# Kernel tuning notes

Hardware: AMD Instinct MI355X
Metric: run time of the kernel (lower is better)

Reference implementation:

```python
import jax, jax.numpy as jnp
import numpy as np
import math

B, S, D, H = 4, 2048, 512, 8
DK = D // H


def setup_inputs() -> dict:
    key = jax.random.key(0)
    ks = jax.random.split(key, 12)
    def lin(k, scale):
        return jax.random.normal(k, (D, D), dtype=jnp.float32) * scale
    s = 1.0 / math.sqrt(D)
    return {
        "q": jax.random.normal(ks[0], (B, S, D), dtype=jnp.float32),
        "k": jax.random.normal(ks[1], (B, S, D), dtype=jnp.float32),
        "v": jax.random.normal(ks[2], (B, S, D), dtype=jnp.float32),
        "mask": jax.random.randint(ks[3], (B, S, S), 0, 2, dtype=jnp.int32),
        "Wq": lin(ks[4], s), "bq": jnp.zeros((D,), jnp.float32),
        "Wk": lin(ks[5], s), "bk": jnp.zeros((D,), jnp.float32),
        "Wv": lin(ks[6], s), "bv": jnp.zeros((D,), jnp.float32),
        "Wo": lin(ks[7], s), "bo": jnp.zeros((D,), jnp.float32),
    }


def reference(q, k, v, mask, Wq, bq, Wk, bk, Wv, bv, Wo, bo):
    bs = q.shape[0]
    # torch Linear: y = x @ W.T + b
    qh = (q @ Wq.T + bq).reshape(bs, -1, H, DK).transpose(0, 2, 1, 3)  # [b,h,s,dk]
    kh = (k @ Wk.T + bk).reshape(bs, -1, H, DK).transpose(0, 2, 1, 3)
    vh = (v @ Wv.T + bv).reshape(bs, -1, H, DK).transpose(0, 2, 1, 3)
    scores = jnp.einsum("bhqd,bhkd->bhqk", qh, kh) / math.sqrt(DK)
    scores = jnp.where(mask[:, None, :, :] == 0, jnp.float32(-1e9), scores)
    scores = jax.nn.softmax(scores, axis=-1)
    # dropout p=0.0 -> identity
    concat = jnp.einsum("bhqk,bhkd->bhqd", scores, vh)
    concat = concat.transpose(0, 2, 1, 3).reshape(bs, -1, D)
    output = concat @ Wo.T + bo
    return (output, scores)
```

## Files before the change

kernel.cpp:

```cpp
#include <hip/hip_runtime.h>
#include <hip/hip_bf16.h>

#define B_ 4
#define S_ 2048
#define D_ 512
#define H_ 8
#define DK_ 64
#define M_ (B_*S_)

typedef float f32x4 __attribute__((ext_vector_type(4)));
typedef __bf16 bf16x8 __attribute__((ext_vector_type(8)));
typedef unsigned short u16x8 __attribute__((ext_vector_type(8)));

static __device__ __forceinline__ unsigned short f2bf(float x) {
    return __builtin_bit_cast(unsigned short, __float2bfloat16(x));
}
static __device__ __forceinline__ float bf2f(unsigned short u) {
    return __bfloat162float(__builtin_bit_cast(__hip_bfloat16, u));
}
static __device__ __forceinline__ bf16x8 ldfrag(const unsigned short* p) {
    return __builtin_bit_cast(bf16x8, *(const u16x8*)p);
}

typedef __attribute__((address_space(1))) const unsigned int gu32;
typedef __attribute__((address_space(3))) unsigned int lu32;
static __device__ __forceinline__ void gl_lds16(const unsigned short* g, unsigned short* l) {
    __builtin_amdgcn_global_load_lds((gu32*)g, (lu32*)l, 16, 0, 0);
}

static __device__ __forceinline__ void split8(const float4 x0, const float4 x1,
                                              u16x8& h, u16x8& l) {
    float f[8] = {x0.x, x0.y, x0.z, x0.w, x1.x, x1.y, x1.z, x1.w};
    #pragma unroll
    for (int j = 0; j < 8; ++j) {
        const unsigned u = __builtin_bit_cast(unsigned, f[j]);
        h[j] = (unsigned short)(u >> 16);
        const float hf = __builtin_bit_cast(float, u & 0xFFFF0000u);
        l[j] = (unsigned short)(__builtin_bit_cast(unsigned, f[j] - hf) >> 16);
    }
}

__global__ __launch_bounds__(256) void split_x3(
    const float* __restrict__ xq, const float* __restrict__ xk, const float* __restrict__ xv,
    unsigned short* __restrict__ qh, unsigned short* __restrict__ qlo,
    unsigned short* __restrict__ kh, unsigned short* __restrict__ klo,
    unsigned short* __restrict__ vh, unsigned short* __restrict__ vlo)
{
    const size_t t = (size_t)blockIdx.x * 256 + threadIdx.x;
    const int z = blockIdx.y;
    const float* in = z == 0 ? xq : z == 1 ? xk : xv;
    unsigned short* oh = z == 0 ? qh : z == 1 ? kh : vh;
    unsigned short* ol = z == 0 ? qlo : z == 1 ? klo : vlo;
    const float4* p = (const float4*)(in + t * 8);
    u16x8 hh, ll;
    split8(p[0], p[1], hh, ll);
    ((u16x8*)oh)[t] = hh;
    ((u16x8*)ol)[t] = ll;
}

__global__ __launch_bounds__(256) void split_w4(
    const float* __restrict__ Wq, const float* __restrict__ Wk,
    const float* __restrict__ Wv, const float* __restrict__ Wo,
    unsigned short* __restrict__ Wcat_h, unsigned short* __restrict__ Wcat_l,
    unsigned short* __restrict__ Wo_h, unsigned short* __restrict__ Wo_l)
{
    const size_t t = (size_t)blockIdx.x * 256 + threadIdx.x;
    const int z = blockIdx.y;
    const float* in = z == 0 ? Wq : z == 1 ? Wk : z == 2 ? Wv : Wo;
    unsigned short* oh = z < 3 ? Wcat_h + (size_t)z * 262144 : Wo_h;
    unsigned short* ol = z < 3 ? Wcat_l + (size_t)z * 262144 : Wo_l;
    const float4* p = (const float4*)(in + t * 8);
    u16x8 hh, ll;
    split8(p[0], p[1], hh, ll);
    ((u16x8*)oh)[t] = hh;
    ((u16x8*)ol)[t] = ll;
}

__global__ __launch_bounds__(256) void mask_pack(
    const int* __restrict__ mask, unsigned long long* __restrict__ bits)
{
    const size_t t = (size_t)blockIdx.x * 256 + threadIdx.x;
    const int m = mask[t];
    const unsigned long long w = __ballot(m != 0);
    if ((threadIdx.x & 63) == 0) bits[t >> 6] = w;
}

__global__ __launch_bounds__(256) void gemm_hl(
    const unsigned short* __restrict__ qXh, const unsigned short* __restrict__ qXl,
    const unsigned short* __restrict__ kXh, const unsigned short* __restrict__ kXl,
    const unsigned short* __restrict__ vXh, const unsigned short* __restrict__ vXl,
    const unsigned short* __restrict__ Wh, const unsigned short* __restrict__ Wl,
    const float* __restrict__ b0, const float* __restrict__ b1, const float* __restrict__ b2,
    float* __restrict__ Yf32,
    unsigned short* __restrict__ q_hi, unsigned short* __restrict__ q_lo,
    unsigned short* __restrict__ k_hi, unsigned short* __restrict__ k_lo,
    unsigned short* __restrict__ v_hi, int fused)
{
    __shared__ unsigned short sAh[128 * 64], sAl[128 * 64];
    __shared__ unsigned short sBh[64 * 64], sBl[64 * 64];

    const int tid = threadIdx.x;
    const int lane = tid & 63, wv = tid >> 6;
    const int quad = lane >> 4, col = lane & 15;
    const int wm = wv >> 1, wn = wv & 1;
    const int m0 = blockIdx.x * 128;
    const int n0g = blockIdx.y * 64;
    const int mat = fused ? (n0g >> 9) : 0;
    const unsigned short* Xh = (!fused || mat == 0) ? qXh : (mat == 1 ? kXh : vXh);
    const unsigned short* Xl = (!fused || mat == 0) ? qXl : (mat == 1 ? kXl : vXl);

    const int lr = lane >> 3;
    const int lc = (lane & 7) * 8;

    f32x4 acc[4][2] = {};

    for (int kt = 0; kt < D_; kt += 64) {
        #pragma unroll
        for (int i = 0; i < 4; ++i) {
            const int row = wv * 32 + i * 8 + lr;
            gl_lds16(Xh + (size_t)(m0 + row) * D_ + kt + lc, sAh + (size_t)(wv * 32 + i * 8) * 64);
            gl_lds16(Xl + (size_t)(m0 + row) * D_ + kt + lc, sAl + (size_t)(wv * 32 + i * 8) * 64);
        }
        #pragma unroll
        for (int i = 0; i < 2; ++i) {
            const int row = wv * 16 + i * 8 + lr;
            gl_lds16(Wh + (size_t)(n0g + row) * D_ + kt + lc, sBh + (size_t)(wv * 16 + i * 8) * 64);
            gl_lds16(Wl + (size_t)(n0g + row) * D_ + kt + lc, sBl + (size_t)(wv * 16 + i * 8) * 64);
        }
        __syncthreads();

        #pragma unroll
        for (int kc = 0; kc < 64; kc += 32) {
            bf16x8 ah[4], al[4], bh[2], bl[2];
            #pragma unroll
            for (int i = 0; i < 4; ++i) {
                ah[i] = ldfrag(&sAh[(wm * 64 + i * 16 + col) * 64 + kc + quad * 8]);
                al[i] = ldfrag(&sAl[(wm * 64 + i * 16 + col) * 64 + kc + quad * 8]);
            }
            #pragma unroll
            for (int j = 0; j < 2; ++j) {
                bh[j] = ldfrag(&sBh[(wn * 32 + j * 16 + col) * 64 + kc + quad * 8]);
                bl[j] = ldfrag(&sBl[(wn * 32 + j * 16 + col) * 64 + kc + quad * 8]);
            }
            #pragma unroll
            for (int i = 0; i < 4; ++i)
                #pragma unroll
                for (int j = 0; j < 2; ++j) {
                    acc[i][j] = __builtin_amdgcn_mfma_f32_16x16x32_bf16(ah[i], bh[j], acc[i][j], 0, 0, 0);
                    acc[i][j] = __builtin_amdgcn_mfma_f32_16x16x32_bf16(al[i], bh[j], acc[i][j], 0, 0, 0);
                    acc[i][j] = __builtin_amdgcn_mfma_f32_16x16x32_bf16(ah[i], bl[j], acc[i][j], 0, 0, 0);
                }
        }
        __syncthreads();
    }

    #pragma unroll
    for (int j = 0; j < 2; ++j) {
        const int ng = n0g + wn * 32 + j * 16 + col;
        const int n = fused ? (ng & 511) : ng;
        const float bias = fused ? (mat == 0 ? b0[n] : mat == 1 ? b1[n] : b2[n]) : b0[n];
        #pragma unroll
        for (int i = 0; i < 4; ++i) {
            #pragma unroll
            for (int r = 0; r < 4; ++r) {
                const int m = m0 + wm * 64 + i * 16 + quad * 4 + r;
                const float vv = acc[i][j][r] + bias;
                if (!fused) {
                    Yf32[(size_t)m * D_ + n] = vv;
                } else {
                    const int bi = m >> 11, si = m & (S_ - 1);
                    const int hh = n >> 6, dk = n & 63;
                    const size_t idx = (((size_t)bi * H_ + hh) * S_ + si) * DK_ + dk;
                    const unsigned short hi = f2bf(vv);
                    if (mat == 0)      { q_hi[idx] = hi; q_lo[idx] = f2bf(vv - bf2f(hi)); }
                    else if (mat == 1) { k_hi[idx] = hi; k_lo[idx] = f2bf(vv - bf2f(hi)); }
                    else               { v_hi[idx] = hi; }
                }
            }
        }
    }
}

__global__ __launch_bounds__(256) void attn_mfma_kernel(
    const unsigned short* __restrict__ q_hi, const unsigned short* __restrict__ q_lo,
    const unsigned short* __restrict__ k_hi, const unsigned short* __restrict__ k_lo,
    const unsigned short* __restrict__ v_hi, const unsigned long long* __restrict__ mbits,
    float* __restrict__ scores,
    unsigned short* __restrict__ ch, unsigned short* __restrict__ cl)
{
    __shared__ __align__(16) unsigned short sKh[64][72], sKl[64][72];
    __shared__ __align__(16) unsigned short sVt[64][72];
    __shared__ __align__(16) unsigned short sP[64][72];

    const int tid = threadIdx.x;
    const int q0 = blockIdx.x * 64;
    const int h = blockIdx.y, b = blockIdx.z;
    const size_t bh = (size_t)b * H_ + h;
    const int wv = tid >> 6, lane = tid & 63, quad = lane >> 4, col = lane & 15;
    const int sr = tid >> 2, sc = (tid & 3) * 16;

    bf16x8 qh[2], ql[2];
    {
        const size_t qb = (bh * S_ + q0 + wv * 16 + col) * DK_;
        qh[0] = ldfrag(q_hi + qb + quad * 8);
        qh[1] = ldfrag(q_hi + qb + 32 + quad * 8);
        ql[0] = ldfrag(q_lo + qb + quad * 8);
        ql[1] = ldfrag(q_lo + qb + 32 + quad * 8);
    }

    const size_t mrow_base = ((size_t)b * S_ + q0 + wv * 16 + quad * 4) * (S_ / 64);

    u16x8 rkh[2], rkl[2], rv[2];
    auto ld_k = [&](int kt) {
        const u16x8* gh = (const u16x8*)(k_hi + (bh * S_ + kt * 64 + sr) * DK_ + sc);
        const u16x8* gl = (const u16x8*)(k_lo + (bh * S_ + kt * 64 + sr) * DK_ + sc);
        rkh[0] = gh[0]; rkh[1] = gh[1]; rkl[0] = gl[0]; rkl[1] = gl[1];
    };
    auto ld_v = [&](int kt) {
        const u16x8* gv = (const u16x8*)(v_hi + (bh * S_ + kt * 64 + sr) * DK_ + sc);
        rv[0] = gv[0]; rv[1] = gv[1];
    };

    auto compute_svals = [&](const unsigned long long* mw, float sv[4][4]) {
        #pragma unroll
        for (int t = 0; t < 4; ++t) {
            f32x4 acc = {0.f, 0.f, 0.f, 0.f};
            #pragma unroll
            for (int kci = 0; kci < 2; ++kci) {
                bf16x8 bhf = ldfrag(&sKh[t * 16 + col][kci * 32 + quad * 8]);
                bf16x8 blf = ldfrag(&sKl[t * 16 + col][kci * 32 + quad * 8]);
                acc = __builtin_amdgcn_mfma_f32_16x16x32_bf16(qh[kci], bhf, acc, 0, 0, 0);
                acc = __builtin_amdgcn_mfma_f32_16x16x32_bf16(qh[kci], blf, acc, 0, 0, 0);
                acc = __builtin_amdgcn_mfma_f32_16x16x32_bf16(ql[kci], bhf, acc, 0, 0, 0);
            }
            #pragma unroll
            for (int r = 0; r < 4; ++r) {
                float s = acc[r] * 0.125f;
                if (!((mw[r] >> (t * 16 + col)) & 1ull)) s = -1e9f;
                sv[t][r] = s;
            }
        }
    };

    float m_run[4], l_run[4];
    #pragma unroll
    for (int r = 0; r < 4; ++r) { m_run[r] = -1e30f; l_run[r] = 0.f; }

    ld_k(0);
    for (int kt = 0; kt < 32; ++kt) {
        __syncthreads();
        *(u16x8*)&sKh[sr][sc] = rkh[0]; *(u16x8*)&sKh[sr][sc + 8] = rkh[1];
        *(u16x8*)&sKl[sr][sc] = rkl[0]; *(u16x8*)&sKl[sr][sc + 8] = rkl[1];
        __syncthreads();
        if (kt < 31) ld_k(kt + 1);
        unsigned long long mw[4];
        #pragma unroll
        for (int r = 0; r < 4; ++r) mw[r] = mbits[mrow_base + (size_t)r * (S_ / 64) + kt];
        float sv[4][4];
        compute_svals(mw, sv);
        #pragma unroll
        for (int r = 0; r < 4; ++r) {
            float tm = fmaxf(fmaxf(sv[0][r], sv[1][r]), fmaxf(sv[2][r], sv[3][r]));
            #pragma unroll
            for (int mm = 1; mm < 16; mm <<= 1) tm = fmaxf(tm, __shfl_xor(tm, mm));
            const float nm = fmaxf(m_run[r], tm);
            float ts = __expf(sv[0][r] - nm) + __expf(sv[1][r] - nm)
                     + __expf(sv[2][r] - nm) + __expf(sv[3][r] - nm);
            #pragma unroll
            for (int mm = 1; mm < 16; mm <<= 1) ts += __shfl_xor(ts, mm);
            l_run[r] = l_run[r] * __expf(m_run[r] - nm) + ts;
            m_run[r] = nm;
        }
    }
    float inv_l[4];
    #pragma unroll
    for (int r = 0; r < 4; ++r) inv_l[r] = 1.f / l_run[r];

    f32x4 oacc[4] = {};
    ld_k(0); ld_v(0);
    for (int kt = 0; kt < 32; ++kt) {
        __syncthreads();
        *(u16x8*)&sKh[sr][sc] = rkh[0]; *(u16x8*)&sKh[sr][sc + 8] = rkh[1];
        *(u16x8*)&sKl[sr][sc] = rkl[0]; *(u16x8*)&sKl[sr][sc + 8] = rkl[1];
        #pragma unroll
        for (int i = 0; i < 8; ++i) { sVt[sc + i][sr] = rv[0][i]; sVt[sc + 8 + i][sr] = rv[1][i]; }
        __syncthreads();
        if (kt < 31) { ld_k(kt + 1); ld_v(kt + 1); }
        unsigned long long mw[4];
        #pragma unroll
        for (int r = 0; r < 4; ++r) mw[r] = mbits[mrow_base + (size_t)r * (S_ / 64) + kt];
        float sv[4][4];
        compute_svals(mw, sv);
        #pragma unroll
        for (int t = 0; t < 4; ++t) {
            #pragma unroll
            for (int r = 0; r < 4; ++r) {
                const int qg = q0 + wv * 16 + quad * 4 + r;
                const int kg = kt * 64 + t * 16 + col;
                const float p = __expf(sv[t][r] - m_run[r]) * inv_l[r];
                scores[(bh * S_ + qg) * S_ + kg] = p;
                sP[wv * 16 + quad * 4 + r][t * 16 + col] = f2bf(p);
            }
        }
        #pragma unroll
        for (int to = 0; to < 4; ++to) {
            #pragma unroll
            for (int kc = 0; kc < 64; kc += 32) {
                bf16x8 a  = ldfrag(&sP[wv * 16 + col][kc + quad * 8]);
                bf16x8 bb = ldfrag(&sVt[to * 16 + col][kc + quad * 8]);
                oacc[to] = __builtin_amdgcn_mfma_f32_16x16x32_bf16(a, bb, oacc[to], 0, 0, 0);
            }
        }
    }

    #pragma unroll
    for (int to = 0; to < 4; ++to) {
        #pragma unroll
        for (int r = 0; r < 4; ++r) {
            const int qg = q0 + wv * 16 + quad * 4 + r;
            const size_t idx = ((size_t)b * S_ + qg) * D_ + h * DK_ + to * 16 + col;
            const float o = oacc[to][r];
            const unsigned short oh16 = f2bf(o);
            ch[idx] = oh16;
            cl[idx] = f2bf(o - bf2f(oh16));
        }
    }
}

extern "C" void kernel_launch(void* const* d_in, const int* in_sizes, int n_in,
                              void* d_out, int out_size, void* d_ws, size_t ws_size,
                              hipStream_t stream) {
    const float* q  = (const float*)d_in[0];
    const float* k  = (const float*)d_in[1];
    const float* v  = (const float*)d_in[2];
    const int* mask = (const int*)d_in[3];
    const float* Wq = (const float*)d_in[4];  const float* bq = (const float*)d_in[5];
    const float* Wk = (const float*)d_in[6];  const float* bk = (const float*)d_in[7];
    const float* Wv = (const float*)d_in[8];  const float* bv = (const float*)d_in[9];
    const float* Wo = (const float*)d_in[10]; const float* bo = (const float*)d_in[11];

    float* out    = (float*)d_out;
    float* scores = out + (size_t)B_ * S_ * D_;

    const size_t NH = (size_t)B_ * H_ * S_ * DK_;
    unsigned short* W = (unsigned short*)d_ws;
    unsigned short* q_hi = W + 0 * NH;
    unsigned short* q_lo = W + 1 * NH;
    unsigned short* k_hi = W + 2 * NH;
    unsigned short* k_lo = W + 3 * NH;
    unsigned short* v_hi = W + 4 * NH;
    unsigned short* qXh = W + 7 * NH;  unsigned short* qXl = W + 8 * NH;
    unsigned short* kXh = W + 9 * NH;  unsigned short* kXl = W + 10 * NH;
    unsigned short* vXh = W + 11 * NH; unsigned short* vXl = W + 12 * NH;
    unsigned short* cat_h = qXh;       unsigned short* cat_l = qXl;
    unsigned short* Wcat_h = W + 13 * NH;
    unsigned short* Wcat_l = Wcat_h + 786432;
    unsigned short* Wo_h   = Wcat_l + 786432;
    unsigned short* Wo_l   = Wo_h + 262144;
    unsigned long long* mbits = (unsigned long long*)(Wo_l + 262144);

    split_x3<<<dim3(2048, 3), 256, 0, stream>>>(q, k, v, qXh, qXl, kXh, kXl, vXh, vXl);
    split_w4<<<dim3(128, 4), 256, 0, stream>>>(Wq, Wk, Wv, Wo, Wcat_h, Wcat_l, Wo_h, Wo_l);
    mask_pack<<<dim3(65536), 256, 0, stream>>>(mask, mbits);

    gemm_hl<<<dim3(64, 24), 256, 0, stream>>>(
        qXh, qXl, kXh, kXl, vXh, vXl, Wcat_h, Wcat_l, bq, bk, bv,
        nullptr, q_hi, q_lo, k_hi, k_lo, v_hi, 1);

    attn_mfma_kernel<<<dim3(S_ / 64, H_, B_), 256, 0, stream>>>(
        q_hi, q_lo, k_hi, k_lo, v_hi, mbits, scores, cat_h, cat_l);

    gemm_hl<<<dim3(64, 8), 256, 0, stream>>>(
        cat_h, cat_l, nullptr, nullptr, nullptr, nullptr, Wo_h, Wo_l, bo, nullptr, nullptr,
        out, nullptr, nullptr, nullptr, nullptr, nullptr, 0);
}
```

Before: 1.030 ms.

## Double-buffer GEMM with 128x128 tiles and coalesce score stores via LDS

The projection GEMM moves to a 128x128 output tile with BK=32. It uses XOR-swizzled, double-buffered LDS staging so the next tile's global-to-LDS copy overlaps the current MFMAs, and raises priority around the MFMA block. In the attention kernel, the fp32 softmax probabilities were scattered to global one element per lane. They are now staged through LDS (aliasing the K buffer) and written as coalesced float4 rows. This adds an extra barrier per key tile, and the larger GEMM tile halves the grid, which can reduce occupancy and wave count.

```diff
diff --git a/kernel.cpp b/kernel.cpp
--- a/kernel.cpp
+++ b/kernel.cpp
@@ -85,7 +85,8 @@
     if ((threadIdx.x & 63) == 0) bits[t >> 6] = w;
 }
 
-__global__ __launch_bounds__(256) void gemm_hl(
+#define GBK 32
+__global__ __launch_bounds__(256, 2) void gemm_hl(
     const unsigned short* __restrict__ qXh, const unsigned short* __restrict__ qXl,
     const unsigned short* __restrict__ kXh, const unsigned short* __restrict__ kXl,
     const unsigned short* __restrict__ vXh, const unsigned short* __restrict__ vXl,
@@ -96,67 +97,73 @@
     unsigned short* __restrict__ k_hi, unsigned short* __restrict__ k_lo,
     unsigned short* __restrict__ v_hi, int fused)
 {
-    __shared__ unsigned short sAh[128 * 64], sAl[128 * 64];
-    __shared__ unsigned short sBh[64 * 64], sBl[64 * 64];
+    __shared__ __align__(16) unsigned short lds[2][4][128 * GBK];
 
     const int tid = threadIdx.x;
     const int lane = tid & 63, wv = tid >> 6;
     const int quad = lane >> 4, col = lane & 15;
     const int wm = wv >> 1, wn = wv & 1;
     const int m0 = blockIdx.x * 128;
-    const int n0g = blockIdx.y * 64;
+    const int n0g = blockIdx.y * 128;
     const int mat = fused ? (n0g >> 9) : 0;
     const unsigned short* Xh = (!fused || mat == 0) ? qXh : (mat == 1 ? kXh : vXh);
     const unsigned short* Xl = (!fused || mat == 0) ? qXl : (mat == 1 ? kXl : vXl);
 
-    const int lr = lane >> 3;
-    const int lc = (lane & 7) * 8;
-
-    f32x4 acc[4][2] = {};
-
-    for (int kt = 0; kt < D_; kt += 64) {
+    const int rsub = lane >> 2;
+    const int csw = (((lane & 3) ^ ((lane >> 3) & 3))) * 8;
+
+    f32x4 acc[4][4] = {};
+
+    auto STAGE = [&](int t, int buf) {
+        const int kt = t * GBK;
+        #pragma unroll
+        for (int i = 0; i < 2; ++i) {
+            const int r0 = wv * 32 + i * 16;
+            gl_lds16(Xh + (size_t)(m0 + r0 + rsub) * D_ + kt + csw, &lds[buf][0][r0 * GBK]);
+            gl_lds16(Xl + (size_t)(m0 + r0 + rsub) * D_ + kt + csw, &lds[buf][1][r0 * GBK]);
+            gl_lds16(Wh + (size_t)(n0g + r0 + rsub) * D_ + kt + csw, &lds[buf][2][r0 * GBK]);
+            gl_lds16(Wl + (size_t)(n0g + r0 + rsub) * D_ + kt + csw, &lds[buf][3][r0 * GBK]);
+        }
+    };
+
+    auto COMPUTE = [&](int buf) {
+        bf16x8 ah[4], al[4], bh[4], bl[4];
         #pragma unroll
         for (int i = 0; i < 4; ++i) {
-            const int row = wv * 32 + i * 8 + lr;
-            gl_lds16(Xh + (size_t)(m0 + row) * D_ + kt + lc, sAh + (size_t)(wv * 32 + i * 8) * 64);
-            gl_lds16(Xl + (size_t)(m0 + row) * D_ + kt + lc, sAl + (size_t)(wv * 32 + i * 8) * 64);
-        }
-        #pragma unroll
-        for (int i = 0; i < 2; ++i) {
-            const int row = wv * 16 + i * 8 + lr;
-            gl_lds16(Wh + (size_t)(n0g + row) * D_ + kt + lc, sBh + (size_t)(wv * 16 + i * 8) * 64);
-            gl_lds16(Wl + (size_t)(n0g + row) * D_ + kt + lc, sBl + (size_t)(wv * 16 + i * 8) * 64);
-        }
-        __syncthreads();
-
-        #pragma unroll
-        for (int kc = 0; kc < 64; kc += 32) {
-            bf16x8 ah[4], al[4], bh[2], bl[2];
-            #pragma unroll
-            for (int i = 0; i < 4; ++i) {
-                ah[i] = ldfrag(&sAh[(wm * 64 + i * 16 + col) * 64 + kc + quad * 8]);
-                al[i] = ldfrag(&sAl[(wm * 64 + i * 16 + col) * 64 + kc + quad * 8]);
-            }
-            #pragma unroll
-            for (int j = 0; j < 2; ++j) {
-                bh[j] = ldfrag(&sBh[(wn * 32 + j * 16 + col) * 64 + kc + quad * 8]);
-                bl[j] = ldfrag(&sBl[(wn * 32 + j * 16 + col) * 64 + kc + quad * 8]);
-            }
-            #pragma unroll
-            for (int i = 0; i < 4; ++i)
-                #pragma unroll
-                for (int j = 0; j < 2; ++j) {
-                    acc[i][j] = __builtin_amdgcn_mfma_f32_16x16x32_bf16(ah[i], bh[j], acc[i][j], 0, 0, 0);
-                    acc[i][j] = __builtin_amdgcn_mfma_f32_16x16x32_bf16(al[i], bh[j], acc[i][j], 0, 0, 0);
-                    acc[i][j] = __builtin_amdgcn_mfma_f32_16x16x32_bf16(ah[i], bl[j], acc[i][j], 0, 0, 0);
-                }
-        }
-        __syncthreads();
+            const int ra = wm * 64 + i * 16 + col;
+            const int ca = (quad ^ ((ra >> 1) & 3)) * 8;
+            ah[i] = ldfrag(&lds[buf][0][ra * GBK + ca]);
+            al[i] = ldfrag(&lds[buf][1][ra * GBK + ca]);
+            const int rb = wn * 64 + i * 16 + col;
+            const int cb = (quad ^ ((rb >> 1) & 3)) * 8;
+            bh[i] = ldfrag(&lds[buf][2][rb * GBK + cb]);
+            bl[i] = ldfrag(&lds[buf][3][rb * GBK + cb]);
+        }
+        __builtin_amdgcn_s_setprio(1);
+        #pragma unroll
+        for (int i = 0; i < 4; ++i)
+            #pragma unroll
+            for (int j = 0; j < 4; ++j) {
+                acc[i][j] = __builtin_amdgcn_mfma_f32_16x16x32_bf16(ah[i], bh[j], acc[i][j], 0, 0, 0);
+                acc[i][j] = __builtin_amdgcn_mfma_f32_16x16x32_bf16(al[i], bh[j], acc[i][j], 0, 0, 0);
+                acc[i][j] = __builtin_amdgcn_mfma_f32_16x16x32_bf16(ah[i], bl[j], acc[i][j], 0, 0, 0);
+            }
+        __builtin_amdgcn_s_setprio(0);
+    };
+
+    STAGE(0, 0);
+    __syncthreads();
+    int cur = 0;
+    for (int t = 0; t < 16; ++t) {
+        if (t < 15) STAGE(t + 1, cur ^ 1);
+        __builtin_amdgcn_sched_barrier(0);
+        COMPUTE(cur);
+        if (t < 15) { __syncthreads(); cur ^= 1; }
     }
 
     #pragma unroll
-    for (int j = 0; j < 2; ++j) {
-        const int ng = n0g + wn * 32 + j * 16 + col;
+    for (int j = 0; j < 4; ++j) {
+        const int ng = n0g + wn * 64 + j * 16 + col;
         const int n = fused ? (ng & 511) : ng;
         const float bias = fused ? (mat == 0 ? b0[n] : mat == 1 ? b1[n] : b2[n]) : b0[n];
         #pragma unroll
@@ -188,7 +195,7 @@
     float* __restrict__ scores,
     unsigned short* __restrict__ ch, unsigned short* __restrict__ cl)
 {
-    __shared__ __align__(16) unsigned short sKh[64][72], sKl[64][72];
+    __shared__ __align__(16) unsigned short sK2[2][64][72];
     __shared__ __align__(16) unsigned short sVt[64][72];
     __shared__ __align__(16) unsigned short sP[64][72];
 
@@ -198,6 +205,8 @@
     const size_t bh = (size_t)b * H_ + h;
     const int wv = tid >> 6, lane = tid & 63, quad = lane >> 4, col = lane & 15;
     const int sr = tid >> 2, sc = (tid & 3) * 16;
+
+    float* sPF = (float*)&sK2[0][0][0];
 
     bf16x8 qh[2], ql[2];
     {
@@ -225,14 +234,16 @@
         #pragma unroll
         for (int t = 0; t < 4; ++t) {
             f32x4 acc = {0.f, 0.f, 0.f, 0.f};
+            __builtin_amdgcn_s_setprio(1);
             #pragma unroll
             for (int kci = 0; kci < 2; ++kci) {
-                bf16x8 bhf = ldfrag(&sKh[t * 16 + col][kci * 32 + quad * 8]);
-                bf16x8 blf = ldfrag(&sKl[t * 16 + col][kci * 32 + quad * 8]);
+                bf16x8 bhf = ldfrag(&sK2[0][t * 16 + col][kci * 32 + quad * 8]);
+                bf16x8 blf = ldfrag(&sK2[1][t * 16 + col][kci * 32 + quad * 8]);
                 acc = __builtin_amdgcn_mfma_f32_16x16x32_bf16(qh[kci], bhf, acc, 0, 0, 0);
                 acc = __builtin_amdgcn_mfma_f32_16x16x32_bf16(qh[kci], blf, acc, 0, 0, 0);
                 acc = __builtin_amdgcn_mfma_f32_16x16x32_bf16(ql[kci], bhf, acc, 0, 0, 0);
             }
+            __builtin_amdgcn_s_setprio(0);
             #pragma unroll
             for (int r = 0; r < 4; ++r) {
                 float s = acc[r] * 0.125f;
@@ -249,8 +260,8 @@
     ld_k(0);
     for (int kt = 0; kt < 32; ++kt) {
         __syncthreads();
-        *(u16x8*)&sKh[sr][sc] = rkh[0]; *(u16x8*)&sKh[sr][sc + 8] = rkh[1];
-        *(u16x8*)&sKl[sr][sc] = rkl[0]; *(u16x8*)&sKl[sr][sc + 8] = rkl[1];
+        *(u16x8*)&sK2[0][sr][sc] = rkh[0]; *(u16x8*)&sK2[0][sr][sc + 8] = rkh[1];
+        *(u16x8*)&sK2[1][sr][sc] = rkl[0]; *(u16x8*)&sK2[1][sr][sc + 8] = rkl[1];
         __syncthreads();
         if (kt < 31) ld_k(kt + 1);
         unsigned long long mw[4];
@@ -280,8 +291,8 @@
     ld_k(0); ld_v(0);
     for (int kt = 0; kt < 32; ++kt) {
         __syncthreads();
-        *(u16x8*)&sKh[sr][sc] = rkh[0]; *(u16x8*)&sKh[sr][sc + 8] = rkh[1];
-        *(u16x8*)&sKl[sr][sc] = rkl[0]; *(u16x8*)&sKl[sr][sc + 8] = rkl[1];
+        *(u16x8*)&sK2[0][sr][sc] = rkh[0]; *(u16x8*)&sK2[0][sr][sc + 8] = rkh[1];
+        *(u16x8*)&sK2[1][sr][sc] = rkl[0]; *(u16x8*)&sK2[1][sr][sc + 8] = rkl[1];
         #pragma unroll
         for (int i = 0; i < 8; ++i) { sVt[sc + i][sr] = rv[0][i]; sVt[sc + 8 + i][sr] = rv[1][i]; }
         __syncthreads();
@@ -291,17 +302,32 @@
         for (int r = 0; r < 4; ++r) mw[r] = mbits[mrow_base + (size_t)r * (S_ / 64) + kt];
         float sv[4][4];
         compute_svals(mw, sv);
+        float pv[4][4];
         #pragma unroll
         for (int t = 0; t < 4; ++t) {
             #pragma unroll
             for (int r = 0; r < 4; ++r) {
-                const int qg = q0 + wv * 16 + quad * 4 + r;
-                const int kg = kt * 64 + t * 16 + col;
                 const float p = __expf(sv[t][r] - m_run[r]) * inv_l[r];
-                scores[(bh * S_ + qg) * S_ + kg] = p;
+                pv[t][r] = p;
                 sP[wv * 16 + quad * 4 + r][t * 16 + col] = f2bf(p);
             }
         }
+        __syncthreads();
+        #pragma unroll
+        for (int t = 0; t < 4; ++t)
+            #pragma unroll
+            for (int r = 0; r < 4; ++r)
+                sPF[(wv * 16 + quad * 4 + r) * 68 + t * 16 + col] = pv[t][r];
+        #pragma unroll
+        for (int rg = 0; rg < 2; ++rg)
+            #pragma unroll
+            for (int hf = 0; hf < 2; ++hf) {
+                const int rl = wv * 16 + rg * 8 + (lane >> 3);
+                const int cf = hf * 32 + (lane & 7) * 4;
+                const float4 pw = *(const float4*)&sPF[rl * 68 + cf];
+                *(float4*)&scores[(bh * S_ + q0 + rl) * S_ + kt * 64 + cf] = pw;
+            }
+        __builtin_amdgcn_s_setprio(1);
         #pragma unroll
         for (int to = 0; to < 4; ++to) {
             #pragma unroll
@@ -311,6 +337,7 @@
                 oacc[to] = __builtin_amdgcn_mfma_f32_16x16x32_bf16(a, bb, oacc[to], 0, 0, 0);
             }
         }
+        __builtin_amdgcn_s_setprio(0);
     }
 
     #pragma unroll
@@ -363,14 +390,14 @@
     split_w4<<<dim3(128, 4), 256, 0, stream>>>(Wq, Wk, Wv, Wo, Wcat_h, Wcat_l, Wo_h, Wo_l);
     mask_pack<<<dim3(65536), 256, 0, stream>>>(mask, mbits);
 
-    gemm_hl<<<dim3(64, 24), 256, 0, stream>>>(
+    gemm_hl<<<dim3(64, 12), 256, 0, stream>>>(
         qXh, qXl, kXh, kXl, vXh, vXl, Wcat_h, Wcat_l, bq, bk, bv,
         nullptr, q_hi, q_lo, k_hi, k_lo, v_hi, 1);
 
     attn_mfma_kernel<<<dim3(S_ / 64, H_, B_), 256, 0, stream>>>(
         q_hi, q_lo, k_hi, k_lo, v_hi, mbits, scores, cat_h, cat_l);
 
-    gemm_hl<<<dim3(64, 8), 256, 0, stream>>>(
+    gemm_hl<<<dim3(64, 4), 256, 0, stream>>>(
         cat_h, cat_l, nullptr, nullptr, nullptr, nullptr, Wo_h, Wo_l, bo, nullptr, nullptr,
         out, nullptr, nullptr, nullptr, nullptr, nullptr, 0);
 }
```

Result: faster. 988.0 us (-4.0%).
